# Kernel tuning notes

Measured on AMD Instinct MI355X. Metric: run time of the kernel, lower is better.

## Reference

```python
import jax, jax.numpy as jnp
import numpy as np

K_LO, K_HI = 5, 3
HAM_LO = jnp.asarray(np.outer(np.hamming(K_LO), np.hamming(K_LO)), dtype=jnp.float32)
HAM_HI = jnp.asarray(np.outer(np.hamming(K_HI), np.hamming(K_HI)), dtype=jnp.float32)


def conv2d(x, w, b, pad):
    y = jax.lax.conv_general_dilated(x, w, (1, 1), [(pad, pad), (pad, pad)],
                                     dimension_numbers=('NCHW', 'OIHW', 'NCHW'))
    return y + b[None, :, None, None]


def kernel_normalizer(mask, k, ham):
    # softmax over k*k, modulate by hamming window, renormalize to sum 1
    n, mc, h, w = mask.shape
    ch = mc // (k * k)
    m = jax.nn.softmax(mask.reshape(n, ch, k * k, h, w), axis=2)
    m = m.reshape(n, ch, k, k, h, w) * ham[None, None, :, :, None, None]
    m = m / m.sum(axis=(2, 3), keepdims=True)
    return m.reshape(n, mc, h, w)


def extract_patches(x, k):
    # (n,c,h,w) -> (n,c,k*k,h,w), zero-padded, row-major kernel order (matches CARAFE)
    n, c, h, w = x.shape
    p = k // 2
    xp = jnp.pad(x, ((0, 0), (0, 0), (p, p), (p, p)))
    return jnp.stack([xp[:, :, i:i + h, j:j + w] for i in range(k) for j in range(k)], axis=2)


def carafe(x, mask, k, group, up):
    # content-aware reassembly: mask is at (h*up, w*up); source pixel = out_pixel // up
    n, c, h, w = x.shape
    cg = c // group
    patches = extract_patches(x, k).reshape(n, group, cg, k * k, h, w)
    if up == 1:
        m = mask.reshape(n, group, k * k, h, w)
        return jnp.einsum('ngckhw,ngkhw->ngchw', patches, m).reshape(n, c, h, w)
    m = mask.reshape(n, group, k * k, h, up, w, up)
    out = jnp.einsum('ngckhw,ngkhuwv->ngchuwv', patches, m)
    return out.reshape(n, c, h * up, w * up)


def _forward(hr_feat, lr_feat, W_hr, b_hr, W_lr, b_lr, W_enc, b_enc, W_enc2, b_enc2):
    chf = conv2d(hr_feat, W_hr, b_hr, 0)
    clf = conv2d(lr_feat, W_lr, b_lr, 0)
    mask_hr_hr = conv2d(chf, W_enc2, b_enc2, 1)
    m_hi = kernel_normalizer(mask_hr_hr, K_HI, HAM_HI)
    chf = 2.0 * chf - carafe(chf, m_hi, K_HI, 1, 1)
    mask_lr_hr = conv2d(chf, W_enc, b_enc, 1)
    m_lo = kernel_normalizer(mask_lr_hr, K_LO, HAM_LO)
    # carafe(up=2) output is already at hr resolution -> F.interpolate(nearest) is identity
    mask_lr_lr = carafe(conv2d(clf, W_enc, b_enc, 1), m_lo, K_LO, 1, 2)
    mask_lr = mask_lr_hr + mask_lr_lr
    m_lo2 = kernel_normalizer(mask_lr, K_LO, HAM_LO)
    mask_hr_lr = carafe(conv2d(clf, W_enc2, b_enc2, 1), m_lo2, K_LO, 1, 2)
    mask_hr = mask_hr_hr + mask_hr_lr
    mask_lr_n = kernel_normalizer(mask_lr, K_LO, HAM_LO)
    lr_out = carafe(lr_feat, mask_lr_n, K_LO, 1, 2)
    mask_hr_n = kernel_normalizer(mask_hr, K_HI, HAM_HI)
    hr_out = 2.0 * hr_feat - carafe(hr_feat, mask_hr_n, K_HI, 1, 1)
    return (mask_lr_n, hr_out, lr_out)


def setup_inputs() -> dict:
    key = jax.random.key(0)
    ks = jax.random.split(key, 10)
    B, CHR, CLR, CC = 2, 256, 256, 64
    H, W = 128, 128
    h, w = H // 2, W // 2
    f32 = jnp.float32
    return {
        'hr_feat': jax.random.normal(ks[0], (B, CHR, H, W), f32),
        'lr_feat': jax.random.normal(ks[1], (B, CLR, h, w), f32),
        'W_hr': jax.random.normal(ks[2], (CC, CHR, 1, 1), f32) * 0.05,
        'b_hr': jnp.zeros((CC,), f32),
        'W_lr': jax.random.normal(ks[3], (CC, CLR, 1, 1), f32) * 0.05,
        'b_lr': jnp.zeros((CC,), f32),
        'W_enc': jax.random.normal(ks[4], (K_LO * K_LO, CC, 3, 3), f32) * 0.001,
        'b_enc': jnp.zeros((K_LO * K_LO,), f32),
        'W_enc2': jax.random.normal(ks[5], (K_HI * K_HI, CC, 3, 3), f32) * 0.001,
        'b_enc2': jnp.zeros((K_HI * K_HI,), f32),
    }


def reference(hr_feat, lr_feat, W_hr, b_hr, W_lr, b_lr, W_enc, b_enc, W_enc2, b_enc2):
    return _forward(hr_feat, lr_feat, W_hr, b_hr, W_lr, b_lr, W_enc, b_enc, W_enc2, b_enc2)
```

## Files before the change

kernel.cpp:

```cpp
#include <hip/hip_runtime.h>

#define HWH 16384
#define HWL 4096
#define WH 128
#define WL 64

__device__ __forceinline__ float ham3v(int t) {
    const float h[3] = {0.08f, 1.0f, 0.08f};
    return h[t / 3] * h[t % 3];
}
__device__ __forceinline__ float ham5v(int t) {
    const float h[5] = {0.08f, 0.54f, 1.0f, 0.54f, 0.08f};
    return h[t / 5] * h[t % 5];
}

template <int K>
__device__ __forceinline__ void normalize_post(float* m) {
    constexpr int K2 = K * K;
    float mx = -1e30f;
#pragma unroll
    for (int k = 0; k < K2; k++) mx = fmaxf(mx, m[k]);
    float s = 0.f;
#pragma unroll
    for (int k = 0; k < K2; k++) {
        float hv = (K == 3) ? ham3v(k) : ham5v(k);
        float e = __expf(m[k] - mx) * hv;
        m[k] = e;
        s += e;
    }
    float inv = 1.f / s;
#pragma unroll
    for (int k = 0; k < K2; k++) m[k] *= inv;
}

template <int K>
__device__ __forceinline__ void normalize_mask(const float* __restrict src, int stride,
                                               float* m) {
#pragma unroll
    for (int k = 0; k < K * K; k++) m[k] = src[(size_t)k * stride];
    normalize_post<K>(m);
}

struct F4 { float x, y, z, w; };
__device__ __forceinline__ F4 ld4u(const float* p) {
    F4 v;
    __builtin_memcpy(&v, p, 16);
    return v;
}

__device__ __forceinline__ float4 add4(float4 a, float4 b) {
    return make_float4(a.x + b.x, a.y + b.y, a.z + b.z, a.w + b.w);
}

__global__ void prep_w_k(const float* __restrict Whr, const float* __restrict Wlr,
                         const float* __restrict Wenc, const float* __restrict Wenc2,
                         float* __restrict wbase) {
    int tid = blockIdx.x * blockDim.x + threadIdx.x;
    int stride = gridDim.x * blockDim.x;
    float* wt_hr = wbase;
    float* wt_lr = wbase + 16384;
    float* wtE = wbase + 32768;
    float* wtE2 = wbase + 51200;
    for (int i = tid; i < 16384; i += stride) {
        int ci = i >> 6, co = i & 63;
        wt_hr[i] = Whr[co * 256 + ci];
        wt_lr[i] = Wlr[co * 256 + ci];
    }
    for (int i = tid; i < 18432; i += stride) {
        int r = i >> 5, co = i & 31;
        int ci = r / 9, t = r % 9;
        wtE[i] = (co < 25) ? Wenc[(co * 64 + ci) * 9 + t] : 0.f;
    }
    for (int i = tid; i < 9216; i += stride) {
        int r = i >> 4, co = i & 15;
        int ci = r / 9, t = r % 9;
        wtE2[i] = (co < 9) ? Wenc2[(co * 64 + ci) * 9 + t] : 0.f;
    }
}

__global__ __launch_bounds__(256) void conv1x1_all_k(
    const float* __restrict hr, const float* __restrict lrf, const float* __restrict wt_hr,
    const float* __restrict wt_lr, const float* __restrict bhr, const float* __restrict blr,
    float* __restrict chf, float* __restrict clf, float* __restrict chf_pB,
    float* __restrict clf_pB, int N) {
    __shared__ float sm[128 * 64];
    const int HALF = (HWH / 64) * N + (HWL / 64) * N;
    int b = blockIdx.x;
    int s = (b >= HALF) ? 1 : 0;
    if (s) b -= HALF;
    const int HRB = (HWH / 64) * N;
    const float *x, *wt, *bias;
    float* y;
    int HWp, n, px0;
    if (b < HRB) {
        x = hr; wt = wt_hr; bias = bhr; HWp = HWH;
        y = s ? chf_pB : chf;
        n = b / (HWH / 64);
        px0 = (b % (HWH / 64)) * 64;
    } else {
        int b2 = b - HRB;
        x = lrf; wt = wt_lr; bias = blr; HWp = HWL;
        y = s ? clf_pB : clf;
        n = b2 / (HWL / 64);
        px0 = (b2 % (HWL / 64)) * 64;
    }
    int ci0 = s * 128;
    const float* xb = x + ((size_t)n * 256 + ci0) * HWp + px0;
    int pl = threadIdx.x & 63;
    int co0 = __builtin_amdgcn_readfirstlane((int)(threadIdx.x >> 6)) * 16;
    for (int e = threadIdx.x; e < 2048; e += 256) {
        int ci = e >> 4, q = e & 15;
        *reinterpret_cast<float4*>(sm + ci * 64 + q * 4) =
            *reinterpret_cast<const float4*>(xb + (size_t)ci * HWp + q * 4);
    }
    __syncthreads();
    float acc[16];
#pragma unroll
    for (int j = 0; j < 16; j++) acc[j] = 0.f;
    const float* wh = wt + (size_t)ci0 * 64 + co0;
#pragma unroll 8
    for (int ci = 0; ci < 128; ci++) {
        float xv = sm[ci * 64 + pl];
        const float* wr = wh + ci * 64;
#pragma unroll
        for (int j = 0; j < 16; j++) acc[j] = fmaf(wr[j], xv, acc[j]);
    }
    float* yb = y + ((size_t)(n * 64 + co0)) * HWp + px0 + pl;
#pragma unroll
    for (int j = 0; j < 16; j++)
        yb[(size_t)j * HWp] = acc[j] + (s ? 0.f : bias[co0 + j]);
}

__global__ void sum_ab_k(float4* __restrict chf, const float4* __restrict chfB,
                         float4* __restrict clf, const float4* __restrict clfB, int N) {
    const int E1 = N * 64 * HWH / 4, E2 = N * 64 * HWL / 4;
    int i = blockIdx.x * 256 + threadIdx.x;
    if (i < E1) {
        chf[i] = add4(chf[i], chfB[i]);
    } else if (i < E1 + E2) {
        int j = i - E1;
        clf[j] = add4(clf[j], clfB[j]);
    }
}

template <int COUT, int CH, int PAD, int LOG2W, int HH, int WW, int NCI>
__device__ __forceinline__ void conv3x3_2px(const float* __restrict x,
                                            const float* __restrict wt,
                                            const float* __restrict bias,
                                            float* __restrict y, int n, int g, int pxh,
                                            int ci0, bool addb) {
    constexpr int HWp = HH * WW;
    int px = pxh * 2;
    int yy = px >> LOG2W, xx = px & (WW - 1);
    int co0 = g * CH;
    float a0[CH], a1[CH];
#pragma unroll
    for (int j = 0; j < CH; j++) { a0[j] = 0.f; a1[j] = 0.f; }
    const float* xb = x + (size_t)(n * 64 + ci0) * HWp;
    const float* wb0 = wt + (size_t)ci0 * 9 * PAD + co0;
    int roff[3];
    bool rv[3];
#pragma unroll
    for (int r = 0; r < 3; r++) {
        int sy = yy + r - 1;
        rv[r] = (sy >= 0) && (sy < HH);
        roff[r] = sy * WW + xx - 1;
    }
    bool lv = (xx > 0), rgv = (xx < WW - 2);
    for (int ci = 0; ci < NCI; ci++) {
        const float* xc = xb + (size_t)ci * HWp;
        const float* w = wb0 + (size_t)ci * 9 * PAD;
#pragma unroll
        for (int r = 0; r < 3; r++) {
            F4 v = ld4u(xc + roff[r]);
            float t0 = (rv[r] && lv) ? v.x : 0.f;
            float t1 = rv[r] ? v.y : 0.f;
            float t2 = rv[r] ? v.z : 0.f;
            float t3 = (rv[r] && rgv) ? v.w : 0.f;
#pragma unroll
            for (int j = 0; j < CH; j++) {
                float w0 = w[(r * 3 + 0) * PAD + j];
                float w1 = w[(r * 3 + 1) * PAD + j];
                float w2 = w[(r * 3 + 2) * PAD + j];
                a0[j] = fmaf(w0, t0, fmaf(w1, t1, fmaf(w2, t2, a0[j])));
                a1[j] = fmaf(w0, t1, fmaf(w1, t2, fmaf(w2, t3, a1[j])));
            }
        }
    }
#pragma unroll
    for (int j = 0; j < CH; j++) {
        int co = co0 + j;
        if (co < COUT) {
            float bv = addb ? bias[co] : 0.f;
            float* op = y + ((size_t)(n * COUT + co)) * HWp + px;
            *reinterpret_cast<float2*>(op) = make_float2(a0[j] + bv, a1[j] + bv);
        }
    }
}

__global__ __launch_bounds__(256) void conv3x3_CGK_k(
    const float* __restrict chf, const float* __restrict clf, const float* __restrict wtE,
    const float* __restrict wtE2, const float* __restrict benc,
    const float* __restrict benc2, float* __restrict mh_P, float* __restrict g_P,
    float* __restrict k_P, int N) {
    const size_t MS = (size_t)N * 9 * HWH, GS = (size_t)N * 25 * HWL,
                 KS = (size_t)N * 9 * HWL;
    const int GBl = 8 * N * 5 * 4, KBl = 8 * N * 2 * 4;
    int b = blockIdx.x;
    if (b < GBl) {
        int pxb = b % 8;
        int n = (b / 8) % N;
        int t = b / (8 * N);
        int g = t % 5, s = t / 5;
        conv3x3_2px<25, 5, 32, 6, WL, WL, 16>(clf, wtE, benc, g_P + s * GS, n, g,
                                              pxb * 256 + (int)threadIdx.x, s * 16, s == 0);
    } else if (b < GBl + KBl) {
        int b2 = b - GBl;
        int pxb = b2 % 8;
        int n = (b2 / 8) % N;
        int t = b2 / (8 * N);
        int g = t % 2, s = t / 2;
        conv3x3_2px<9, 5, 16, 6, WL, WL, 16>(clf, wtE2, benc2, k_P + s * KS, n, g,
                                             pxb * 256 + (int)threadIdx.x, s * 16, s == 0);
    } else {
        int b3 = b - GBl - KBl;
        int pxb = b3 % 32;
        int n = (b3 / 32) % N;
        int t = b3 / (32 * N);
        int g = t % 3, s = t / 3;
        conv3x3_2px<9, 3, 16, 7, WH, WH, 16>(chf, wtE2, benc2, mh_P + s * MS, n, g,
                                             pxb * 256 + (int)threadIdx.x, s * 16, s == 0);
    }
}

__global__ __launch_bounds__(256) void conv3x3_F_k(const float* __restrict chf2,
                                                   const float* __restrict wtE,
                                                   const float* __restrict benc,
                                                   float* __restrict mlr_P, int N) {
    const size_t FS = (size_t)N * 25 * HWH;
    int t = blockIdx.x;
    int pxb = t % 32; t /= 32;
    int n = t % N; t /= N;
    int g = t % 5;
    int s = t / 5;
    conv3x3_2px<25, 5, 32, 7, WH, WH, 16>(chf2, wtE, benc, mlr_P + s * FS, n, g,
                                          pxb * 256 + (int)threadIdx.x, s * 16, s == 0);
}

__global__ void sum4n_gkc_k(const float* __restrict mh_P, float* __restrict mh_sum,
                            float* __restrict mh_n, const float4* __restrict g,
                            float4* __restrict g_d, const float4* __restrict k,
                            float4* __restrict k_d, int N) {
    const int NA = N * HWH / 256;
    const int E2 = N * 25 * HWL / 4, E3 = N * 9 * HWL / 4;
    const int NB = E2 / 256, NC = E3 / 256;
    const size_t MS = (size_t)N * 9 * HWH;
    int b = blockIdx.x;
    if (b < NA) {
        int lin = b * 256 + threadIdx.x;
        int n = lin / HWH, px = lin % HWH;
        float m[9];
#pragma unroll
        for (int c = 0; c < 9; c++) {
            size_t o = ((size_t)n * 9 + c) * HWH + px;
            float s = mh_P[o] + mh_P[o + MS] + mh_P[o + 2 * MS] + mh_P[o + 3 * MS];
            m[c] = s;
            mh_sum[o] = s;
        }
        normalize_post<3>(m);
#pragma unroll
        for (int c = 0; c < 9; c++) mh_n[((size_t)n * 9 + c) * HWH + px] = m[c];
    } else if (b < NA + NB) {
        int i = (b - NA) * 256 + threadIdx.x;
        if (i < E2) g_d[i] = add4(add4(g[i], g[i + E2]), add4(g[i + 2 * E2], g[i + 3 * E2]));
    } else {
        int i = (b - NA - NB) * 256 + threadIdx.x;
        if (i < E3) k_d[i] = add4(add4(k[i], k[i + E3]), add4(k[i + 2 * E3], k[i + 3 * E3]));
    }
}

__global__ void sum4_f_k(const float4* __restrict p, float4* __restrict d, int N) {
    const int E = N * 25 * HWH / 4;
    int i = blockIdx.x * 256 + threadIdx.x;
    if (i < E) d[i] = add4(add4(p[i], p[i + E]), add4(p[i + 2 * E], p[i + 3 * E]));
}

template <int NCH>
__device__ __forceinline__ void stage_tile136(const float* __restrict src,
                                              float (*__restrict tile)[10][136], int y0) {
    int tid = threadIdx.x;
    if (tid < 80) {
        int r = tid >> 3, c8 = tid & 7;
        int col = (c8 < 4) ? c8 : 128 + c8;
#pragma unroll
        for (int c = 0; c < NCH; c++) tile[c][r][col] = 0.f;
    }
    int r0 = tid >> 5, q0 = tid & 31;
    int gy0 = y0 + r0 - 1;
    bool v0 = (gy0 >= 0) && (gy0 < WH);
    int e1 = tid + 256;
    int r1 = e1 >> 5, q1 = e1 & 31;
    int gy1 = e1 < 320 ? (y0 + r1 - 1) : 0;
    bool v1 = (e1 < 320) && (y0 + r1 - 1 >= 0) && (y0 + r1 - 1 < WH);
#pragma unroll
    for (int c = 0; c < NCH; c++) {
        const float* sp = src + (size_t)c * HWH;
        float4 a = make_float4(0.f, 0.f, 0.f, 0.f);
        if (v0) a = *(const float4*)(sp + gy0 * WH + q0 * 4);
        *(float4*)&tile[c][r0][4 + q0 * 4] = a;
        if (e1 < 320) {
            float4 bb = make_float4(0.f, 0.f, 0.f, 0.f);
            if (v1) bb = *(const float4*)(sp + gy1 * WH + q1 * 4);
            *(float4*)&tile[c][r1][4 + q1 * 4] = bb;
        }
    }
    __syncthreads();
}

template <int NCH, bool SUBTRACT>
__device__ __forceinline__ void carafe3_tile(const float (*__restrict tile)[10][136],
                                             const float* __restrict mb, int y0,
                                             float* __restrict ob) {
    int ly = threadIdx.x >> 5;
    int x0 = (threadIdx.x & 31) * 4;
    int px = (y0 + ly) * WH + x0;
    float4 m4[9];
#pragma unroll
    for (int t = 0; t < 9; t++) m4[t] = *(const float4*)(mb + (size_t)t * HWH + px);
    for (int c = 0; c < NCH; c++) {
        float row[3][6];
#pragma unroll
        for (int r = 0; r < 3; r++) {
            float lft = tile[c][ly + r][3 + x0];
            float4 mid = *(const float4*)&tile[c][ly + r][4 + x0];
            float rgt = tile[c][ly + r][8 + x0];
            row[r][0] = lft; row[r][1] = mid.x; row[r][2] = mid.y; row[r][3] = mid.z;
            row[r][4] = mid.w; row[r][5] = rgt;
        }
        float4 res;
        float* rp = &res.x;
#pragma unroll
        for (int p = 0; p < 4; p++) {
            float s = 0.f;
#pragma unroll
            for (int r = 0; r < 3; r++)
#pragma unroll
                for (int cc = 0; cc < 3; cc++)
                    s = fmaf(((const float*)&m4[r * 3 + cc])[p], row[r][p + cc], s);
            rp[p] = SUBTRACT ? (2.f * row[1][p + 1] - s) : s;
        }
        *(float4*)(ob + (size_t)c * HWH + px) = res;
    }
}

__global__ __launch_bounds__(256) void fuse_de_k(const float* __restrict chf,
                                                 const float* __restrict m9n,
                                                 float* __restrict chf2, int N) {
    __shared__ float tile[8][10][136];
    int b = blockIdx.x;
    int yt = b & 15;
    int g = (b >> 4) & 7;
    int n = b >> 7;
    int y0 = yt * 8;
    int c0 = g * 8;
    stage_tile136<8>(chf + ((size_t)n * 64 + c0) * HWH, tile, y0);
    carafe3_tile<8, true>(tile, m9n + (size_t)n * 9 * HWH, y0,
                          chf2 + ((size_t)n * 64 + c0) * HWH);
}

__global__ void fuse_hi_k(const float* __restrict m, const float* __restrict g,
                          float* __restrict mask_lr, int N) {
    int b = blockIdx.x;
    int pxb = b % 64;
    int n = (b / 64) % N;
    int co0 = (b / (64 * N)) * 5;
    int px = pxb * 256 + threadIdx.x;
    int Y = px >> 7, X = px & 127;
    int h = Y >> 1, w = X >> 1;
    const float* mb = m + (size_t)n * 25 * HWH + px;
    float ml[25];
    normalize_mask<5>(mb, HWH, ml);
    float acc[5];
#pragma unroll
    for (int j = 0; j < 5; j++) acc[j] = 0.f;
    const float* gb = g + ((size_t)n * 25 + co0) * HWL;
    for (int k = 0; k < 25; k++) {
        int sy = h + k / 5 - 2, sx = w + k % 5 - 2;
        if (sy >= 0 && sy < WL && sx >= 0 && sx < WL) {
            int off = sy * WL + sx;
            float mk = ml[k];
#pragma unroll
            for (int j = 0; j < 5; j++)
                acc[j] = fmaf(mk, gb[(size_t)j * HWL + off], acc[j]);
        }
    }
#pragma unroll
    for (int j = 0; j < 5; j++)
        mask_lr[((size_t)(n * 25 + co0 + j)) * HWH + px] =
            mb[(size_t)(co0 + j) * HWH] + acc[j];
}

__global__ void fuse_l_norm_k(const float* __restrict mask_lr, const float* __restrict kf,
                              const float* __restrict mh_sum, float* __restrict out0,
                              float* __restrict mask_hr_n, int N) {
    int b = blockIdx.x;
    int px = (b % 256) * 64 + threadIdx.x;
    int n = b / 256;
    int Y = px >> 7, X = px & 127;
    int h = Y >> 1, w = X >> 1;
    float ml[25];
    normalize_mask<5>(mask_lr + (size_t)n * 25 * HWH + px, HWH, ml);
    float* op = out0 + (size_t)n * 25 * HWH + px;
#pragma unroll
    for (int k = 0; k < 25; k++) op[(size_t)k * HWH] = ml[k];
    float acc[9];
#pragma unroll
    for (int j = 0; j < 9; j++) acc[j] = 0.f;
    const float* kb = kf + (size_t)n * 9 * HWL;
    for (int k = 0; k < 25; k++) {
        int sy = h + k / 5 - 2, sx = w + k % 5 - 2;
        if (sy >= 0 && sy < WL && sx >= 0 && sx < WL) {
            int off = sy * WL + sx;
            float mk = ml[k];
#pragma unroll
            for (int j = 0; j < 9; j++)
                acc[j] = fmaf(mk, kb[(size_t)j * HWL + off], acc[j]);
        }
    }
    float mh[9];
#pragma unroll
    for (int j = 0; j < 9; j++)
        mh[j] = mh_sum[((size_t)(n * 9 + j)) * HWH + px] + acc[j];
    normalize_post<3>(mh);
    float* dp = mask_hr_n + (size_t)n * 9 * HWH + px;
#pragma unroll
    for (int j = 0; j < 9; j++) dp[(size_t)j * HWH] = mh[j];
}

#define HRCHG 8
__global__ __launch_bounds__(256) void hr_out_k(const float* __restrict m9n,
                                                const float* __restrict hr,
                                                float* __restrict out1, int N) {
    __shared__ float tile[HRCHG][10][136];
    int b = blockIdx.x;
    int yt = b & 15;
    int g = (b >> 4) & 31;
    int n = b >> 9;
    int y0 = yt * 8;
    int c0 = g * HRCHG;
    stage_tile136<HRCHG>(hr + ((size_t)n * 256 + c0) * HWH, tile, y0);
    carafe3_tile<HRCHG, true>(tile, m9n + (size_t)n * 9 * HWH, y0,
                              out1 + ((size_t)n * 256 + c0) * HWH);
}

#define LRCHG 8
__global__ __launch_bounds__(256) void lr_out_k(const float* __restrict m_n,
                                                const float* __restrict lr,
                                                float* __restrict out2, int N) {
    __shared__ float tile[LRCHG][12][68];
    int b = blockIdx.x;
    int yt = b & 7;
    int g = (b >> 3) & 31;
    int n = b >> 8;
    int y0 = yt * 16;
    int hbase = y0 >> 1;
    int c0 = g * LRCHG;
    const float* lrb = lr + ((size_t)n * 256 + c0) * HWL;
    if (threadIdx.x < 48) {
        int r = threadIdx.x >> 2, c4 = threadIdx.x & 3;
        int col = (c4 < 2) ? c4 : 64 + c4;
#pragma unroll
        for (int c = 0; c < LRCHG; c++) tile[c][r][col] = 0.f;
    }
#pragma unroll
    for (int c = 0; c < LRCHG; c++) {
        const float* sp = lrb + (size_t)c * HWL;
#pragma unroll
        for (int p = 0; p < 2; p++) {
            int e = threadIdx.x + p * 256;
            if (e < 384) {
                int r = e >> 5, q = e & 31;
                int h = hbase + r - 2;
                float2 v = make_float2(0.f, 0.f);
                if (h >= 0 && h < WL) v = *(const float2*)(sp + h * WL + q * 2);
                *(float2*)&tile[c][r][2 + q * 2] = v;
            }
        }
    }
    __syncthreads();
    const float* mb = m_n + (size_t)n * 25 * HWH;
    float* ob = out2 + ((size_t)n * 256 + c0) * HWH;
#pragma unroll
    for (int i = 0; i < 2; i++) {
        int q = threadIdx.x + 256 * i;
        int qy = q >> 6, qx = q & 63;
        int Y0 = y0 + 2 * qy;
        int X0 = 2 * qx;
        float2 mk0[25], mk1[25];
#pragma unroll
        for (int k = 0; k < 25; k++) {
            mk0[k] = *(const float2*)(mb + (size_t)k * HWH + Y0 * WH + X0);
            mk1[k] = *(const float2*)(mb + (size_t)k * HWH + (Y0 + 1) * WH + X0);
        }
        for (int c = 0; c < LRCHG; c++) {
            float a00 = 0.f, a01 = 0.f, a10 = 0.f, a11 = 0.f;
#pragma unroll
            for (int k = 0; k < 25; k++) {
                float v = tile[c][qy + k / 5][qx + k % 5];
                a00 = fmaf(mk0[k].x, v, a00);
                a01 = fmaf(mk0[k].y, v, a01);
                a10 = fmaf(mk1[k].x, v, a10);
                a11 = fmaf(mk1[k].y, v, a11);
            }
            float* op = ob + (size_t)c * HWH + (size_t)Y0 * WH + X0;
            *(float2*)op = make_float2(a00, a01);
            *(float2*)(op + WH) = make_float2(a10, a11);
        }
    }
}

extern "C" void kernel_launch(void* const* d_in, const int* in_sizes, int n_in, void* d_out,
                              int out_size, void* d_ws, size_t ws_size, hipStream_t stream) {
    const float* hr = (const float*)d_in[0];
    const float* lr = (const float*)d_in[1];
    const float* Whr = (const float*)d_in[2];
    const float* bhr = (const float*)d_in[3];
    const float* Wlr = (const float*)d_in[4];
    const float* blr = (const float*)d_in[5];
    const float* Wenc = (const float*)d_in[6];
    const float* benc = (const float*)d_in[7];
    const float* Wenc2 = (const float*)d_in[8];
    const float* benc2 = (const float*)d_in[9];
    float* out = (float*)d_out;
    const int B = in_sizes[0] / (256 * HWH);
    (void)d_ws; (void)ws_size;

    float* out0 = out;
    float* O1 = out + (size_t)B * 25 * HWH;
    float* O2 = O1 + (size_t)B * 256 * HWH;

    const size_t MS = (size_t)B * 9 * HWH;
    const size_t GS = (size_t)B * 25 * HWL;
    const size_t KS = (size_t)B * 9 * HWL;
    const size_t FS = (size_t)B * 25 * HWH;

    float* wbase = O2;
    float* wt_hr = wbase;
    float* wt_lr = wbase + 16384;
    float* wtE = wbase + 32768;
    float* wtE2 = wbase + 51200;
    float* mh_P = O2 + 60416;
    float* g_P = mh_P + 4 * MS;
    float* k_P = g_P + 4 * GS;
    float* m_hrhr_sum = k_P + 4 * KS;
    float* g_sum = m_hrhr_sum + MS;
    float* k_sum = g_sum + GS;
    float* m_lrhr_sum = k_sum + KS;
    float* mask_hr_n = m_lrhr_sum + FS;
    float* chf_pB = mask_hr_n + MS;
    float* clf_pB = chf_pB + (size_t)B * 64 * HWH;

    float* chf = O1;
    float* chf2 = chf + (size_t)B * 64 * HWH;
    float* clf = chf2 + (size_t)B * 64 * HWH;
    float* mlr_P = clf + (size_t)B * 64 * HWL;
    float* m_hrhr_n = mlr_P + 4 * FS;
    float* mask_lr = mlr_P;

    prep_w_k<<<64, 256, 0, stream>>>(Whr, Wlr, Wenc, Wenc2, wbase);
    conv1x1_all_k<<<((HWH / 64) * B + (HWL / 64) * B) * 2, 256, 0, stream>>>(
        hr, lr, wt_hr, wt_lr, bhr, blr, chf, clf, chf_pB, clf_pB, B);
    sum_ab_k<<<(B * 64 * (HWH + HWL) / 4 + 255) / 256, 256, 0, stream>>>(
        (float4*)chf, (const float4*)chf_pB, (float4*)clf, (const float4*)clf_pB, B);
    conv3x3_CGK_k<<<8 * B * 5 * 4 + 8 * B * 2 * 4 + 32 * B * 3 * 4, 256, 0, stream>>>(
        chf, clf, wtE, wtE2, benc, benc2, mh_P, g_P, k_P, B);
    {
        int NA = B * HWH / 256;
        int NB = (B * 25 * HWL / 4) / 256, NC = (B * 9 * HWL / 4) / 256;
        sum4n_gkc_k<<<NA + NB + NC, 256, 0, stream>>>(
            mh_P, m_hrhr_sum, m_hrhr_n, (const float4*)g_P, (float4*)g_sum,
            (const float4*)k_P, (float4*)k_sum, B);
    }
    fuse_de_k<<<B * 128, 256, 0, stream>>>(chf, m_hrhr_n, chf2, B);
    conv3x3_F_k<<<32 * B * 5 * 4, 256, 0, stream>>>(chf2, wtE, benc, mlr_P, B);
    sum4_f_k<<<((int)FS / 4 + 255) / 256, 256, 0, stream>>>((const float4*)mlr_P,
                                                            (float4*)m_lrhr_sum, B);
    fuse_hi_k<<<64 * B * 5, 256, 0, stream>>>(m_lrhr_sum, g_sum, mask_lr, B);
    fuse_l_norm_k<<<256 * B, 64, 0, stream>>>(mask_lr, k_sum, m_hrhr_sum, out0, mask_hr_n,
                                              B);
    hr_out_k<<<B * 512, 256, 0, stream>>>(mask_hr_n, hr, O1, B);
    lr_out_k<<<B * 256, 256, 0, stream>>>(out0, lr, O2, B);
}
```

Baseline: 160.5 us.

## Drop split-K in 1x1 conv and enlarge CARAFE3 tiles to 16 rows by 8 px

The 1x1 convolution no longer splits the 256 input channels across two blocks. Each block now loops over both halves in shared memory, which removes the partial-sum buffers and the separate sum_ab kernel launch. The 3x3 CARAFE tile kernels (fuse_de_k, hr_out_k) now stage 16 rows by 4 channels and have each thread compute 8 pixels instead of 4. This amortizes the mask loads and halo reads over more work. The trade-off is half as many blocks for the 1x1 conv, a longer serial loop per block, and more registers per thread in CARAFE.

```diff
diff --git a/kernel.cpp b/kernel.cpp
--- a/kernel.cpp
+++ b/kernel.cpp
@@ -81,66 +81,51 @@
 __global__ __launch_bounds__(256) void conv1x1_all_k(
     const float* __restrict hr, const float* __restrict lrf, const float* __restrict wt_hr,
     const float* __restrict wt_lr, const float* __restrict bhr, const float* __restrict blr,
-    float* __restrict chf, float* __restrict clf, float* __restrict chf_pB,
-    float* __restrict clf_pB, int N) {
+    float* __restrict chf, float* __restrict clf, int N) {
     __shared__ float sm[128 * 64];
-    const int HALF = (HWH / 64) * N + (HWL / 64) * N;
-    int b = blockIdx.x;
-    int s = (b >= HALF) ? 1 : 0;
-    if (s) b -= HALF;
+    int b = blockIdx.x;
     const int HRB = (HWH / 64) * N;
     const float *x, *wt, *bias;
     float* y;
     int HWp, n, px0;
     if (b < HRB) {
-        x = hr; wt = wt_hr; bias = bhr; HWp = HWH;
-        y = s ? chf_pB : chf;
+        x = hr; wt = wt_hr; bias = bhr; y = chf; HWp = HWH;
         n = b / (HWH / 64);
         px0 = (b % (HWH / 64)) * 64;
     } else {
         int b2 = b - HRB;
-        x = lrf; wt = wt_lr; bias = blr; HWp = HWL;
-        y = s ? clf_pB : clf;
+        x = lrf; wt = wt_lr; bias = blr; y = clf; HWp = HWL;
         n = b2 / (HWL / 64);
         px0 = (b2 % (HWL / 64)) * 64;
     }
-    int ci0 = s * 128;
-    const float* xb = x + ((size_t)n * 256 + ci0) * HWp + px0;
+    const float* xb = x + (size_t)n * 256 * HWp + px0;
     int pl = threadIdx.x & 63;
     int co0 = __builtin_amdgcn_readfirstlane((int)(threadIdx.x >> 6)) * 16;
-    for (int e = threadIdx.x; e < 2048; e += 256) {
-        int ci = e >> 4, q = e & 15;
-        *reinterpret_cast<float4*>(sm + ci * 64 + q * 4) =
-            *reinterpret_cast<const float4*>(xb + (size_t)ci * HWp + q * 4);
-    }
-    __syncthreads();
     float acc[16];
 #pragma unroll
     for (int j = 0; j < 16; j++) acc[j] = 0.f;
-    const float* wh = wt + (size_t)ci0 * 64 + co0;
+    const float* w0 = wt + co0;
+#pragma unroll
+    for (int half = 0; half < 2; half++) {
+        __syncthreads();
+        for (int e = threadIdx.x; e < 2048; e += 256) {
+            int ci = e >> 4, q = e & 15;
+            *reinterpret_cast<float4*>(sm + ci * 64 + q * 4) =
+                *reinterpret_cast<const float4*>(xb + (size_t)(half * 128 + ci) * HWp + q * 4);
+        }
+        __syncthreads();
+        const float* wh = w0 + (half * 128) * 64;
 #pragma unroll 8
-    for (int ci = 0; ci < 128; ci++) {
-        float xv = sm[ci * 64 + pl];
-        const float* wr = wh + ci * 64;
-#pragma unroll
-        for (int j = 0; j < 16; j++) acc[j] = fmaf(wr[j], xv, acc[j]);
+        for (int ci = 0; ci < 128; ci++) {
+            float xv = sm[ci * 64 + pl];
+            const float* wr = wh + ci * 64;
+#pragma unroll
+            for (int j = 0; j < 16; j++) acc[j] = fmaf(wr[j], xv, acc[j]);
+        }
     }
     float* yb = y + ((size_t)(n * 64 + co0)) * HWp + px0 + pl;
 #pragma unroll
-    for (int j = 0; j < 16; j++)
-        yb[(size_t)j * HWp] = acc[j] + (s ? 0.f : bias[co0 + j]);
-}
-
-__global__ void sum_ab_k(float4* __restrict chf, const float4* __restrict chfB,
-                         float4* __restrict clf, const float4* __restrict clfB, int N) {
-    const int E1 = N * 64 * HWH / 4, E2 = N * 64 * HWL / 4;
-    int i = blockIdx.x * 256 + threadIdx.x;
-    if (i < E1) {
-        chf[i] = add4(chf[i], chfB[i]);
-    } else if (i < E1 + E2) {
-        int j = i - E1;
-        clf[j] = add4(clf[j], clfB[j]);
-    }
+    for (int j = 0; j < 16; j++) yb[(size_t)j * HWp] = acc[j] + bias[co0 + j];
 }
 
 template <int COUT, int CH, int PAD, int LOG2W, int HH, int WW, int NCI>
@@ -253,7 +238,7 @@
                             float4* __restrict k_d, int N) {
     const int NA = N * HWH / 256;
     const int E2 = N * 25 * HWL / 4, E3 = N * 9 * HWL / 4;
-    const int NB = E2 / 256, NC = E3 / 256;
+    const int NB = E2 / 256;
     const size_t MS = (size_t)N * 9 * HWH;
     int b = blockIdx.x;
     if (b < NA) {
@@ -285,87 +270,96 @@
     if (i < E) d[i] = add4(add4(p[i], p[i + E]), add4(p[i + 2 * E], p[i + 3 * E]));
 }
 
-template <int NCH>
-__device__ __forceinline__ void stage_tile136(const float* __restrict src,
-                                              float (*__restrict tile)[10][136], int y0) {
+__device__ __forceinline__ void stage_tile18(const float* __restrict src,
+                                             float (*__restrict tile)[18][136], int y0) {
     int tid = threadIdx.x;
-    if (tid < 80) {
+    if (tid < 144) {
         int r = tid >> 3, c8 = tid & 7;
         int col = (c8 < 4) ? c8 : 128 + c8;
 #pragma unroll
-        for (int c = 0; c < NCH; c++) tile[c][r][col] = 0.f;
-    }
-    int r0 = tid >> 5, q0 = tid & 31;
-    int gy0 = y0 + r0 - 1;
-    bool v0 = (gy0 >= 0) && (gy0 < WH);
-    int e1 = tid + 256;
-    int r1 = e1 >> 5, q1 = e1 & 31;
-    int gy1 = e1 < 320 ? (y0 + r1 - 1) : 0;
-    bool v1 = (e1 < 320) && (y0 + r1 - 1 >= 0) && (y0 + r1 - 1 < WH);
-#pragma unroll
-    for (int c = 0; c < NCH; c++) {
+        for (int c = 0; c < 4; c++) tile[c][r][col] = 0.f;
+    }
+#pragma unroll
+    for (int c = 0; c < 4; c++) {
         const float* sp = src + (size_t)c * HWH;
-        float4 a = make_float4(0.f, 0.f, 0.f, 0.f);
-        if (v0) a = *(const float4*)(sp + gy0 * WH + q0 * 4);
-        *(float4*)&tile[c][r0][4 + q0 * 4] = a;
-        if (e1 < 320) {
-            float4 bb = make_float4(0.f, 0.f, 0.f, 0.f);
-            if (v1) bb = *(const float4*)(sp + gy1 * WH + q1 * 4);
-            *(float4*)&tile[c][r1][4 + q1 * 4] = bb;
+#pragma unroll
+        for (int p = 0; p < 3; p++) {
+            int e = tid + p * 256;
+            if (e < 576) {
+                int r = e >> 5, q = e & 31;
+                int gy = y0 + r - 1;
+                float4 v = make_float4(0.f, 0.f, 0.f, 0.f);
+                if (gy >= 0 && gy < WH) v = *(const float4*)(sp + gy * WH + q * 4);
+                *(float4*)&tile[c][r][4 + q * 4] = v;
+            }
         }
     }
     __syncthreads();
 }
 
-template <int NCH, bool SUBTRACT>
-__device__ __forceinline__ void carafe3_tile(const float (*__restrict tile)[10][136],
-                                             const float* __restrict mb, int y0,
-                                             float* __restrict ob) {
-    int ly = threadIdx.x >> 5;
-    int x0 = (threadIdx.x & 31) * 4;
+template <bool SUBTRACT>
+__device__ __forceinline__ void carafe3_tile8(const float (*__restrict tile)[18][136],
+                                              const float* __restrict mb, int y0,
+                                              float* __restrict ob) {
+    int ly = threadIdx.x >> 4;
+    int x0 = (threadIdx.x & 15) * 8;
     int px = (y0 + ly) * WH + x0;
-    float4 m4[9];
-#pragma unroll
-    for (int t = 0; t < 9; t++) m4[t] = *(const float4*)(mb + (size_t)t * HWH + px);
-    for (int c = 0; c < NCH; c++) {
-        float row[3][6];
+    float4 ma[9], mbv[9];
+#pragma unroll
+    for (int t = 0; t < 9; t++) {
+        ma[t] = *(const float4*)(mb + (size_t)t * HWH + px);
+        mbv[t] = *(const float4*)(mb + (size_t)t * HWH + px + 4);
+    }
+    for (int c = 0; c < 4; c++) {
+        float row[3][10];
 #pragma unroll
         for (int r = 0; r < 3; r++) {
-            float lft = tile[c][ly + r][3 + x0];
-            float4 mid = *(const float4*)&tile[c][ly + r][4 + x0];
-            float rgt = tile[c][ly + r][8 + x0];
-            row[r][0] = lft; row[r][1] = mid.x; row[r][2] = mid.y; row[r][3] = mid.z;
-            row[r][4] = mid.w; row[r][5] = rgt;
-        }
-        float4 res;
-        float* rp = &res.x;
-#pragma unroll
-        for (int p = 0; p < 4; p++) {
+            const float* tp = &tile[c][ly + r][0];
+            float lft = tp[3 + x0];
+            float4 m0 = *(const float4*)&tp[4 + x0];
+            float4 m1 = *(const float4*)&tp[8 + x0];
+            float rgt = tp[12 + x0];
+            row[r][0] = lft;
+            row[r][1] = m0.x; row[r][2] = m0.y; row[r][3] = m0.z; row[r][4] = m0.w;
+            row[r][5] = m1.x; row[r][6] = m1.y; row[r][7] = m1.z; row[r][8] = m1.w;
+            row[r][9] = rgt;
+        }
+        float4 resA, resB;
+        float* rp = &resA.x;
+        float* rq = &resB.x;
+#pragma unroll
+        for (int p = 0; p < 8; p++) {
             float s = 0.f;
 #pragma unroll
             for (int r = 0; r < 3; r++)
 #pragma unroll
-                for (int cc = 0; cc < 3; cc++)
-                    s = fmaf(((const float*)&m4[r * 3 + cc])[p], row[r][p + cc], s);
-            rp[p] = SUBTRACT ? (2.f * row[1][p + 1] - s) : s;
-        }
-        *(float4*)(ob + (size_t)c * HWH + px) = res;
+                for (int cc = 0; cc < 3; cc++) {
+                    float mv = (p < 4) ? ((const float*)&ma[r * 3 + cc])[p]
+                                       : ((const float*)&mbv[r * 3 + cc])[p - 4];
+                    s = fmaf(mv, row[r][p + cc], s);
+                }
+            float o = SUBTRACT ? (2.f * row[1][p + 1] - s) : s;
+            if (p < 4) rp[p] = o; else rq[p - 4] = o;
+        }
+        float* op = ob + (size_t)c * HWH + px;
+        *(float4*)op = resA;
+        *(float4*)(op + 4) = resB;
     }
 }
 
 __global__ __launch_bounds__(256) void fuse_de_k(const float* __restrict chf,
                                                  const float* __restrict m9n,
                                                  float* __restrict chf2, int N) {
-    __shared__ float tile[8][10][136];
-    int b = blockIdx.x;
-    int yt = b & 15;
-    int g = (b >> 4) & 7;
+    __shared__ float tile[4][18][136];
+    int b = blockIdx.x;
+    int yt = b & 7;
+    int g = (b >> 3) & 15;
     int n = b >> 7;
-    int y0 = yt * 8;
-    int c0 = g * 8;
-    stage_tile136<8>(chf + ((size_t)n * 64 + c0) * HWH, tile, y0);
-    carafe3_tile<8, true>(tile, m9n + (size_t)n * 9 * HWH, y0,
-                          chf2 + ((size_t)n * 64 + c0) * HWH);
+    int y0 = yt * 16;
+    int c0 = g * 4;
+    stage_tile18(chf + ((size_t)n * 64 + c0) * HWH, tile, y0);
+    carafe3_tile8<true>(tile, m9n + (size_t)n * 9 * HWH, y0,
+                        chf2 + ((size_t)n * 64 + c0) * HWH);
 }
 
 __global__ void fuse_hi_k(const float* __restrict m, const float* __restrict g,
@@ -437,20 +431,19 @@
     for (int j = 0; j < 9; j++) dp[(size_t)j * HWH] = mh[j];
 }
 
-#define HRCHG 8
 __global__ __launch_bounds__(256) void hr_out_k(const float* __restrict m9n,
                                                 const float* __restrict hr,
                                                 float* __restrict out1, int N) {
-    __shared__ float tile[HRCHG][10][136];
-    int b = blockIdx.x;
-    int yt = b & 15;
-    int g = (b >> 4) & 31;
+    __shared__ float tile[4][18][136];
+    int b = blockIdx.x;
+    int yt = b & 7;
+    int g = (b >> 3) & 63;
     int n = b >> 9;
-    int y0 = yt * 8;
-    int c0 = g * HRCHG;
-    stage_tile136<HRCHG>(hr + ((size_t)n * 256 + c0) * HWH, tile, y0);
-    carafe3_tile<HRCHG, true>(tile, m9n + (size_t)n * 9 * HWH, y0,
-                              out1 + ((size_t)n * 256 + c0) * HWH);
+    int y0 = yt * 16;
+    int c0 = g * 4;
+    stage_tile18(hr + ((size_t)n * 256 + c0) * HWH, tile, y0);
+    carafe3_tile8<true>(tile, m9n + (size_t)n * 9 * HWH, y0,
+                        out1 + ((size_t)n * 256 + c0) * HWH);
 }
 
 #define LRCHG 8
@@ -557,8 +550,6 @@
     float* k_sum = g_sum + GS;
     float* m_lrhr_sum = k_sum + KS;
     float* mask_hr_n = m_lrhr_sum + FS;
-    float* chf_pB = mask_hr_n + MS;
-    float* clf_pB = chf_pB + (size_t)B * 64 * HWH;
 
     float* chf = O1;
     float* chf2 = chf + (size_t)B * 64 * HWH;
@@ -568,10 +559,8 @@
     float* mask_lr = mlr_P;
 
     prep_w_k<<<64, 256, 0, stream>>>(Whr, Wlr, Wenc, Wenc2, wbase);
-    conv1x1_all_k<<<((HWH / 64) * B + (HWL / 64) * B) * 2, 256, 0, stream>>>(
-        hr, lr, wt_hr, wt_lr, bhr, blr, chf, clf, chf_pB, clf_pB, B);
-    sum_ab_k<<<(B * 64 * (HWH + HWL) / 4 + 255) / 256, 256, 0, stream>>>(
-        (float4*)chf, (const float4*)chf_pB, (float4*)clf, (const float4*)clf_pB, B);
+    conv1x1_all_k<<<(HWH / 64) * B + (HWL / 64) * B, 256, 0, stream>>>(
+        hr, lr, wt_hr, wt_lr, bhr, blr, chf, clf, B);
     conv3x3_CGK_k<<<8 * B * 5 * 4 + 8 * B * 2 * 4 + 32 * B * 3 * 4, 256, 0, stream>>>(
         chf, clf, wtE, wtE2, benc, benc2, mh_P, g_P, k_P, B);
     {
```

New measurement: 157.0 us. 1.02x faster.
